# Performance work log

Hardware: AMD Instinct MI355X
Metric: run time of the kernel (lower is better)

The kernel has to match this reference:

```python
import jax, jax.numpy as jnp
import numpy as np

N_IN = 2048
N_OUT = 2048
RANK = 64
NUM_ITER = 4  # Newton-Schulz iterations, matches default num_iter=4


def setup_inputs() -> dict:
    key = jax.random.key(0)
    k1, k2, k3 = jax.random.split(key, 3)
    # scale U,V modestly so A = UV^T - VU^T is well-conditioned (mimics orthogonal init scale)
    scale = 1.0 / np.sqrt(N_IN)
    return {
        "input": jax.random.normal(k1, (8, 2048, N_IN), dtype=jnp.float32),
        "U": jax.random.normal(k2, (N_IN, RANK), dtype=jnp.float32) * scale,
        "V": jax.random.normal(k3, (N_IN, RANK), dtype=jnp.float32) * scale,
    }


def _orthogonal_weight(U, V):
    # A = U V^T - V U^T  (skew-symmetric, rank <= 2*rank)
    A = U @ V.T - V @ U.T              # [n, n]
    I = jnp.eye(N_IN, dtype=A.dtype)
    B = I - A
    X = I
    for _ in range(NUM_ITER):          # Newton-Schulz iteration for B^{-1}
        X = X @ (2.0 * I - B @ X)
    W_square = (I + A) @ X             # Cayley transform (I+A)(I-A)^{-1} approx
    return W_square[:N_OUT, :N_IN]


def reference(input, U, V):
    W = _orthogonal_weight(U, V)       # [out, in]
    # F.linear(input, W) = input @ W.T
    return jnp.einsum("bsi,oi->bso", input, W)
```

## Files before the change

### kernel.cpp

```cpp
#include <hip/hip_runtime.h>
#include <hip/hip_bf16.h>
#include <cstdint>
#include <cstddef>

#define NIN   2048
#define RANK  64
#define R2    128
#define NROWS 16384

typedef __bf16 bf16x8 __attribute__((ext_vector_type(8)));
typedef float  f32x4  __attribute__((ext_vector_type(4)));
typedef unsigned short u16x8 __attribute__((ext_vector_type(8)));

__device__ __forceinline__ unsigned short f2bf(float f) {
  union { float f; unsigned u; } x; x.f = f;
  return (unsigned short)((x.u + 0x7fffu + ((x.u >> 16) & 1u)) >> 16);
}

__global__ void k_zero(float* __restrict__ G) {
  G[blockIdx.x * 256 + threadIdx.x] = 0.f;
}

__global__ void k_prep(const float* __restrict__ U, const float* __restrict__ V,
                       unsigned short* __restrict__ Mf, float* __restrict__ G) {
  int b = blockIdx.x, tid = threadIdx.x;
  if (b < 128) {
    int CI = b * 256 + tid;
    int lane = CI & 63, J = (CI >> 6) & 63, t = CI >> 12;
    int n = t * 16 + (lane & 15);
    int k0 = J * 32 + (lane >> 4) * 8;
    const float* src = (n < RANK) ? (U + n) : (V + (n - RANK));
    u16x8 h;
#pragma unroll
    for (int e = 0; e < 8; ++e) h[e] = f2bf(src[(size_t)(k0 + e) * RANK]);
    *(u16x8*)(Mf + (size_t)CI * 8) = h;
  }
  int tile = b >> 3, ks = b & 7;
  int bi = tile >> 3, bj = tile & 7;
  int ty = tid >> 4, tx = tid & 15;
  int i = bi * 16 + ty, j = bj * 16 + tx;
  const float* Ai = (i < RANK) ? (U + i) : (V + (i - RANK));
  const float* Aj = (j < RANK) ? (U + j) : (V + (j - RANK));
  int k0 = ks * 256;
  float acc = 0.f;
#pragma unroll 8
  for (int k = k0; k < k0 + 256; ++k) acc += Ai[(size_t)k * RANK] * Aj[(size_t)k * RANK];
  if (i < RANK) atomicAdd(&G[(i + RANK) * R2 + j], -acc);
  else          atomicAdd(&G[(i - RANK) * R2 + j],  acc);
}

struct SOp { const float* A; const float* B; float* O; float a, b; };
struct SOps { SOp op[3]; };
__global__ void k_small(SOps ops) {
  SOp o = ops.op[blockIdx.x >> 6];
  int t = blockIdx.x & 63;
  int i = (t >> 3) * 16 + (threadIdx.x >> 4);
  int j = (t & 7) * 16 + (threadIdx.x & 15);
  float acc = 0.f;
#pragma unroll 8
  for (int k = 0; k < R2; ++k) {
    float av = o.A[i * R2 + k]; if (k == i) av += o.a;
    float bv = o.B[k * R2 + j]; if (k == j) bv += o.b;
    acc += av * bv;
  }
  o.O[i * R2 + j] = acc;
}

__global__ void k_D(const float* __restrict__ U, const float* __restrict__ V,
                    const float* __restrict__ H, const float* __restrict__ G15,
                    unsigned short* __restrict__ Df) {
  int idx = blockIdx.x * 256 + threadIdx.x;
  int i = idx >> 7, j = idx & 127;
  int jj = (j < RANK) ? (j + RANK) : (j - RANK);
  float sgn = (j < RANK) ? -1.f : 1.f;
  float acc = 0.f;
#pragma unroll 8
  for (int k = 0; k < R2; ++k) {
    float m = (k < RANK) ? U[(size_t)i * RANK + k] : V[(size_t)i * RANK + (k - RANK)];
    float t = 2.f * H[k * R2 + jj] - G15[k * R2 + jj];
    acc += m * (sgn * t);
  }
  int t_ = i >> 4, lr = i & 15;
  int J = j >> 5, lg = (j >> 3) & 3, e = j & 7;
  size_t CI = (size_t)(t_ * 4 + J) * 64 + lg * 16 + lr;
  Df[CI * 8 + e] = f2bf(acc);
}

__global__ __launch_bounds__(256) void k_T1(const float* __restrict__ input,
                                            const unsigned short* __restrict__ Mf,
                                            unsigned short* __restrict__ T1bf) {
  __shared__ __align__(16) unsigned char lds[73728];
  const int tid = threadIdx.x, lane = tid & 63, w = tid >> 6;
  const int lr = lane & 15, lg = lane >> 4;
  const int row0 = blockIdx.x * 32;
  unsigned char* abuf = lds + w * 8192;
  float* rbuf = (float*)lds;

  f32x4 acc[2][8] = {};
  const float* gbase = input + (size_t)row0 * NIN + w * 512;
  const int Jbase = w * 16;

  float4 s0[8], s1[8];
  bf16x8 bx[8], by[8];

#define T1_SLOAD(KT)                                                          \
  _Pragma("unroll") for (int p = 0; p < 8; ++p) {                             \
    int id = p * 64 + lane; int r = id >> 4, C = id & 15;                     \
    const float* g = gbase + (size_t)r * NIN + (KT) * 128 + C * 8;            \
    s0[p] = *(const float4*)g; s1[p] = *(const float4*)(g + 4);               \
  }
#define T1_SWRITE()                                                           \
  _Pragma("unroll") for (int p = 0; p < 8; ++p) {                             \
    int id = p * 64 + lane; int r = id >> 4, C = id & 15;                     \
    u16x8 h;                                                                  \
    h[0] = f2bf(s0[p].x); h[1] = f2bf(s0[p].y);                               \
    h[2] = f2bf(s0[p].z); h[3] = f2bf(s0[p].w);                               \
    h[4] = f2bf(s1[p].x); h[5] = f2bf(s1[p].y);                               \
    h[6] = f2bf(s1[p].z); h[7] = f2bf(s1[p].w);                               \
    *(u16x8*)(abuf + r * 256 + ((C ^ (r & 7)) << 4)) = h;                     \
  }
#define T1_BLOAD(P, S)                                                        \
  _Pragma("unroll") for (int t = 0; t < 8; ++t)                               \
    P[t] = *(const bf16x8*)(Mf + ((size_t)(t * 64 + Jbase + (S)) * 64 + lane) * 8);

  T1_SLOAD(0);
  T1_SWRITE();
  T1_BLOAD(bx, 0);

#pragma unroll
  for (int s = 0; s < 16; ++s) {
    const int kt = s >> 2, j = s & 3;
    if (j == 0 && kt < 3) { T1_SLOAD(kt + 1); }
    bf16x8 a0, a1;
    {
      int C = j * 4 + lg;
      a0 = *(const bf16x8*)(abuf + lr * 256 + ((C ^ (lr & 7)) << 4));
      a1 = *(const bf16x8*)(abuf + (16 + lr) * 256 + ((C ^ ((16 + lr) & 7)) << 4));
    }
    if (s < 15) { if (s & 1) { T1_BLOAD(bx, s + 1); } else { T1_BLOAD(by, s + 1); } }
#pragma unroll
    for (int t = 0; t < 8; ++t) {
      bf16x8 bcur = (s & 1) ? by[t] : bx[t];
      acc[0][t] = __builtin_amdgcn_mfma_f32_16x16x32_bf16(a0, bcur, acc[0][t], 0, 0, 0);
      acc[1][t] = __builtin_amdgcn_mfma_f32_16x16x32_bf16(a1, bcur, acc[1][t], 0, 0, 0);
    }
    if (j == 3 && kt < 3) { T1_SWRITE(); }
  }

  __syncthreads();
#pragma unroll
  for (int m = 0; m < 2; ++m)
#pragma unroll
    for (int t = 0; t < 8; ++t) {
      int col = t * 16 + lr, row = m * 16 + lg * 4;
      *(f32x4*)&rbuf[((size_t)w * 128 + col) * 36 + row] = acc[m][t];
    }
  __syncthreads();
  {
    int r = tid & 31, cg = tid >> 5;
    u16x8 o1, o2;
#pragma unroll
    for (int i = 0; i < 16; ++i) {
      int col = cg * 16 + i;
      float s = rbuf[(size_t)col * 36 + r]
              + rbuf[((size_t)128 + col) * 36 + r]
              + rbuf[((size_t)256 + col) * 36 + r]
              + rbuf[((size_t)384 + col) * 36 + r];
      if (i < 8) o1[i] = f2bf(s); else o2[i - 8] = f2bf(s);
    }
    unsigned short* dst = T1bf + (size_t)(row0 + r) * R2 + cg * 16;
    *(u16x8*)dst = o1;
    *(u16x8*)(dst + 8) = o2;
  }
}

__global__ __launch_bounds__(256) void k_OUT(const float* __restrict__ input,
                                             const unsigned short* __restrict__ T1bf,
                                             const unsigned short* __restrict__ Df,
                                             float* __restrict__ out) {
  __shared__ float obuf[4][32][132];
  const int tid = threadIdx.x, lane = tid & 63, w = tid >> 6;
  const int lr = lane & 15, lg = lane >> 4;
  const int row0 = blockIdx.x * 32;

  bf16x8 bq[2][4];
#pragma unroll
  for (int R = 0; R < 2; ++R)
#pragma unroll
    for (int J = 0; J < 4; ++J)
      bq[R][J] = *(const bf16x8*)(T1bf + (size_t)(row0 + R * 16 + lr) * R2 + J * 32 + lg * 8);

  bf16x8 xd[4], yd[4];
#define O_DLOAD(P, TTI)                                                       \
  _Pragma("unroll") for (int J = 0; J < 4; ++J)                               \
    P[J] = *(const bf16x8*)(Df + ((size_t)((w * 32 + (TTI)) * 4 + J) * 64 + lane) * 8);

  O_DLOAD(xd, 0);
#pragma unroll
  for (int g = 0; g < 4; ++g) {
#pragma unroll
    for (int tt = 0; tt < 8; ++tt) {
      const int tti = g * 8 + tt;
      if (tti < 31) { if (tti & 1) { O_DLOAD(xd, tti + 1); } else { O_DLOAD(yd, tti + 1); } }
#pragma unroll
      for (int R = 0; R < 2; ++R) {
        f32x4 o = {};
#pragma unroll
        for (int J = 0; J < 4; ++J) {
          bf16x8 d = (tti & 1) ? yd[J] : xd[J];
          o = __builtin_amdgcn_mfma_f32_16x16x32_bf16(d, bq[R][J], o, 0, 0, 0);
        }
        *(f32x4*)&obuf[w][R * 16 + lr][tt * 16 + lg * 4] = o;
      }
    }
#pragma unroll
    for (int c = 0; c < 16; ++c) {
      int id = c * 64 + lane;
      int r = id >> 5, cc = id & 31;
      f32x4 v = *(const f32x4*)&obuf[w][r][cc * 4];
      int grow = row0 + r, gcol = w * 512 + g * 128 + cc * 4;
      float4 inv = *(const float4*)(input + (size_t)grow * NIN + gcol);
      float4 res = { v[0] + inv.x, v[1] + inv.y, v[2] + inv.z, v[3] + inv.w };
      *(float4*)(out + (size_t)grow * NIN + gcol) = res;
    }
  }
}

extern "C" void kernel_launch(void* const* d_in, const int* in_sizes, int n_in,
                              void* d_out, int out_size, void* d_ws, size_t ws_size,
                              hipStream_t stream) {
  const float* input = (const float*)d_in[0];
  const float* U     = (const float*)d_in[1];
  const float* V     = (const float*)d_in[2];
  float* out = (float*)d_out;
  char* ws = (char*)d_ws;

  float* mats = (float*)ws;
  float* G   = mats + 0 * 16384;
  float* G2  = mats + 1 * 16384;
  float* G3  = mats + 2 * 16384;
  float* G4  = mats + 3 * 16384;
  float* G7  = mats + 4 * 16384;
  float* G8  = mats + 5 * 16384;
  float* H12 = mats + 6 * 16384;
  float* H124= mats + 7 * 16384;
  float* H   = mats + 8 * 16384;
  float* G15 = mats + 9 * 16384;
  unsigned short* Mf   = (unsigned short*)(ws + 10 * 65536);
  unsigned short* Df   = (unsigned short*)(ws + 10 * 65536 + 524288);
  unsigned short* T1bf = (unsigned short*)(ws + 10 * 65536 + 2 * 524288);

  k_zero<<<64, 256, 0, stream>>>(G);
  k_prep<<<512, 256, 0, stream>>>(U, V, Mf, G);
  k_T1<<<512, 256, 0, stream>>>(input, Mf, T1bf);

  { SOps o = {{ {G,  G,  G2, 0.f, 0.f}, {nullptr,nullptr,nullptr,0.f,0.f}, {nullptr,nullptr,nullptr,0.f,0.f} }};
    k_small<<<64, 256, 0, stream>>>(o); }
  { SOps o = {{ {G2, G2, G4, 0.f, 0.f}, {G2, G, G3, 0.f, 0.f}, {G, G2, H12, 1.f, 1.f} }};
    k_small<<<192, 256, 0, stream>>>(o); }
  { SOps o = {{ {G4, G4, G8, 0.f, 0.f}, {G3, G4, G7, 0.f, 0.f}, {H12, G4, H124, 0.f, 1.f} }};
    k_small<<<192, 256, 0, stream>>>(o); }
  { SOps o = {{ {G7, G8, G15, 0.f, 0.f}, {H124, G8, H, 0.f, 1.f}, {nullptr,nullptr,nullptr,0.f,0.f} }};
    k_small<<<128, 256, 0, stream>>>(o); }

  k_D<<<1024, 256, 0, stream>>>(U, V, H, G15, Df);
  k_OUT<<<512, 256, 0, stream>>>(input, T1bf, Df, out);
}
```

Before: 140.6 us.

## Fuse small-GEMM chain via grid barriers and merge T1 with output GEMM

```diff
diff --git a/kernel.cpp b/kernel.cpp
--- a/kernel.cpp
+++ b/kernel.cpp
@@ -17,8 +17,9 @@
   return (unsigned short)((x.u + 0x7fffu + ((x.u >> 16) & 1u)) >> 16);
 }
 
-__global__ void k_zero(float* __restrict__ G) {
+__global__ void k_zero(float* __restrict__ G, int* __restrict__ cnt) {
   G[blockIdx.x * 256 + threadIdx.x] = 0.f;
+  if (blockIdx.x == 0 && threadIdx.x < 8) cnt[threadIdx.x] = 0;
 }
 
 __global__ void k_prep(const float* __restrict__ U, const float* __restrict__ V,
@@ -49,46 +50,111 @@
   else          atomicAdd(&G[(i - RANK) * R2 + j],  acc);
 }
 
-struct SOp { const float* A; const float* B; float* O; float a, b; };
-struct SOps { SOp op[3]; };
-__global__ void k_small(SOps ops) {
-  SOp o = ops.op[blockIdx.x >> 6];
-  int t = blockIdx.x & 63;
-  int i = (t >> 3) * 16 + (threadIdx.x >> 4);
-  int j = (t & 7) * 16 + (threadIdx.x & 15);
+__device__ __forceinline__ void smallGemm(const float* __restrict__ A,
+                                          const float* __restrict__ B,
+                                          float* __restrict__ O,
+                                          float a, float b, int t, int tid) {
+  int i = (t >> 3) * 16 + (tid >> 4);
+  int j = (t & 7) * 16 + (tid & 15);
   float acc = 0.f;
 #pragma unroll 8
   for (int k = 0; k < R2; ++k) {
-    float av = o.A[i * R2 + k]; if (k == i) av += o.a;
-    float bv = o.B[k * R2 + j]; if (k == j) bv += o.b;
+    float av = A[i * R2 + k]; if (k == i) av += a;
+    float bv = B[k * R2 + j]; if (k == j) bv += b;
     acc += av * bv;
   }
-  o.O[i * R2 + j] = acc;
-}
-
-__global__ void k_D(const float* __restrict__ U, const float* __restrict__ V,
-                    const float* __restrict__ H, const float* __restrict__ G15,
-                    unsigned short* __restrict__ Df) {
-  int idx = blockIdx.x * 256 + threadIdx.x;
-  int i = idx >> 7, j = idx & 127;
-  int jj = (j < RANK) ? (j + RANK) : (j - RANK);
-  float sgn = (j < RANK) ? -1.f : 1.f;
-  float acc = 0.f;
-#pragma unroll 8
-  for (int k = 0; k < R2; ++k) {
-    float m = (k < RANK) ? U[(size_t)i * RANK + k] : V[(size_t)i * RANK + (k - RANK)];
-    float t = 2.f * H[k * R2 + jj] - G15[k * R2 + jj];
-    acc += m * (sgn * t);
-  }
-  int t_ = i >> 4, lr = i & 15;
-  int J = j >> 5, lg = (j >> 3) & 3, e = j & 7;
-  size_t CI = (size_t)(t_ * 4 + J) * 64 + lg * 16 + lr;
-  Df[CI * 8 + e] = f2bf(acc);
-}
-
-__global__ __launch_bounds__(256) void k_T1(const float* __restrict__ input,
-                                            const unsigned short* __restrict__ Mf,
-                                            unsigned short* __restrict__ T1bf) {
+  O[i * R2 + j] = acc;
+}
+
+__device__ __forceinline__ void gbar(int* c, int target, int tid) {
+  __syncthreads();
+  if (tid == 0) {
+    __threadfence();
+    __hip_atomic_fetch_add(c, 1, __ATOMIC_RELEASE, __HIP_MEMORY_SCOPE_AGENT);
+  }
+  while (__hip_atomic_load(c, __ATOMIC_ACQUIRE, __HIP_MEMORY_SCOPE_AGENT) < target)
+    __builtin_amdgcn_s_sleep(8);
+}
+
+__global__ __launch_bounds__(256) void k_chainD(const float* __restrict__ U,
+                                                const float* __restrict__ V,
+                                                float* __restrict__ mats,
+                                                unsigned short* __restrict__ Df,
+                                                int* __restrict__ cnt) {
+  __shared__ float elds[16384];
+  float* G_   = mats;
+  float* G2_  = mats + 1 * 16384;
+  float* G3_  = mats + 2 * 16384;
+  float* G4_  = mats + 3 * 16384;
+  float* G7_  = mats + 4 * 16384;
+  float* G8_  = mats + 5 * 16384;
+  float* H12_ = mats + 6 * 16384;
+  float* H124_= mats + 7 * 16384;
+  float* H_   = mats + 8 * 16384;
+  float* G15_ = mats + 9 * 16384;
+  const int cb = blockIdx.x, tid = threadIdx.x;
+
+  if (cb < 64) smallGemm(G_, G_, G2_, 0.f, 0.f, cb, tid);
+  gbar(&cnt[0], 192, tid);
+  { int op = cb >> 6, t = cb & 63;
+    if (op == 0)      smallGemm(G2_, G2_, G4_,  0.f, 0.f, t, tid);
+    else if (op == 1) smallGemm(G2_, G_,  G3_,  0.f, 0.f, t, tid);
+    else              smallGemm(G_,  G2_, H12_, 1.f, 1.f, t, tid); }
+  gbar(&cnt[1], 192, tid);
+  { int op = cb >> 6, t = cb & 63;
+    if (op == 0)      smallGemm(G4_,  G4_, G8_,   0.f, 0.f, t, tid);
+    else if (op == 1) smallGemm(G3_,  G4_, G7_,   0.f, 0.f, t, tid);
+    else              smallGemm(H12_, G4_, H124_, 0.f, 1.f, t, tid); }
+  gbar(&cnt[2], 192, tid);
+  if (cb < 128) {
+    int op = cb >> 6, t = cb & 63;
+    if (op == 0) smallGemm(G7_,   G8_, G15_, 0.f, 0.f, t, tid);
+    else         smallGemm(H124_, G8_, H_,   0.f, 1.f, t, tid);
+  }
+  gbar(&cnt[3], 192, tid);
+
+  if (cb < 128) {
+    const float4* H4 = (const float4*)H_;
+    const float4* X4 = (const float4*)G15_;
+#pragma unroll
+    for (int it = 0; it < 16; ++it) {
+      int i4 = it * 256 + tid;
+      float4 h = H4[i4], x = X4[i4];
+      float4 e = { 2.f*h.x - x.x, 2.f*h.y - x.y, 2.f*h.z - x.z, 2.f*h.w - x.w };
+      ((float4*)elds)[i4] = e;
+    }
+    __syncthreads();
+    int j = tid & 127, half = tid >> 7;
+    int jj = (j < RANK) ? (j + RANK) : (j - RANK);
+    float sgn = (j < RANK) ? -1.f : 1.f;
+    int i0 = cb * 16 + half * 8;
+    float acc[8] = {};
+#pragma unroll 4
+    for (int k = 0; k < RANK; ++k) {
+      float e = sgn * elds[k * R2 + jj];
+#pragma unroll
+      for (int rr = 0; rr < 8; ++rr) acc[rr] += U[(i0 + rr) * RANK + k] * e;
+    }
+#pragma unroll 4
+    for (int k = 0; k < RANK; ++k) {
+      float e = sgn * elds[(k + RANK) * R2 + jj];
+#pragma unroll
+      for (int rr = 0; rr < 8; ++rr) acc[rr] += V[(i0 + rr) * RANK + k] * e;
+    }
+#pragma unroll
+    for (int rr = 0; rr < 8; ++rr) {
+      int i = i0 + rr;
+      int t_ = i >> 4, lr = i & 15, J = j >> 5, lg = (j >> 3) & 3, e8 = j & 7;
+      size_t CI = (size_t)(t_ * 4 + J) * 64 + lg * 16 + lr;
+      Df[CI * 8 + e8] = f2bf(acc[rr]);
+    }
+  }
+}
+
+__global__ __launch_bounds__(256) void k_main(const float* __restrict__ input,
+                                              const unsigned short* __restrict__ Mf,
+                                              const unsigned short* __restrict__ Df,
+                                              float* __restrict__ out) {
   __shared__ __align__(16) unsigned char lds[73728];
   const int tid = threadIdx.x, lane = tid & 63, w = tid >> 6;
   const int lr = lane & 15, lg = lane >> 4;
@@ -99,7 +165,6 @@
   f32x4 acc[2][8] = {};
   const float* gbase = input + (size_t)row0 * NIN + w * 512;
   const int Jbase = w * 16;
-
   float4 s0[8], s1[8];
   bf16x8 bx[8], by[8];
 
@@ -126,7 +191,6 @@
   T1_SLOAD(0);
   T1_SWRITE();
   T1_BLOAD(bx, 0);
-
 #pragma unroll
   for (int s = 0; s < 16; ++s) {
     const int kt = s >> 2, j = s & 3;
@@ -158,38 +222,33 @@
   __syncthreads();
   {
     int r = tid & 31, cg = tid >> 5;
-    u16x8 o1, o2;
+    float sums[16];
 #pragma unroll
     for (int i = 0; i < 16; ++i) {
       int col = cg * 16 + i;
-      float s = rbuf[(size_t)col * 36 + r]
+      sums[i] = rbuf[(size_t)col * 36 + r]
               + rbuf[((size_t)128 + col) * 36 + r]
               + rbuf[((size_t)256 + col) * 36 + r]
               + rbuf[((size_t)384 + col) * 36 + r];
-      if (i < 8) o1[i] = f2bf(s); else o2[i - 8] = f2bf(s);
-    }
-    unsigned short* dst = T1bf + (size_t)(row0 + r) * R2 + cg * 16;
-    *(u16x8*)dst = o1;
-    *(u16x8*)(dst + 8) = o2;
-  }
-}
-
-__global__ __launch_bounds__(256) void k_OUT(const float* __restrict__ input,
-                                             const unsigned short* __restrict__ T1bf,
-                                             const unsigned short* __restrict__ Df,
-                                             float* __restrict__ out) {
-  __shared__ float obuf[4][32][132];
-  const int tid = threadIdx.x, lane = tid & 63, w = tid >> 6;
-  const int lr = lane & 15, lg = lane >> 4;
-  const int row0 = blockIdx.x * 32;
+    }
+    __syncthreads();
+    u16x8 o1, o2;
+#pragma unroll
+    for (int i = 0; i < 8; ++i) { o1[i] = f2bf(sums[i]); o2[i] = f2bf(sums[8 + i]); }
+    *(u16x8*)(lds + 65536 + r * 256 + (((cg * 2)     ^ (r & 7)) << 4)) = o1;
+    *(u16x8*)(lds + 65536 + r * 256 + (((cg * 2 + 1) ^ (r & 7)) << 4)) = o2;
+  }
+  __syncthreads();
 
   bf16x8 bq[2][4];
 #pragma unroll
   for (int R = 0; R < 2; ++R)
 #pragma unroll
-    for (int J = 0; J < 4; ++J)
-      bq[R][J] = *(const bf16x8*)(T1bf + (size_t)(row0 + R * 16 + lr) * R2 + J * 32 + lg * 8);
-
+    for (int J = 0; J < 4; ++J) {
+      int row = R * 16 + lr, cc = J * 4 + lg;
+      bq[R][J] = *(const bf16x8*)(lds + 65536 + row * 256 + ((cc ^ (row & 7)) << 4));
+    }
+  float* obufw = (float*)(lds + w * 8704);
   bf16x8 xd[4], yd[4];
 #define O_DLOAD(P, TTI)                                                       \
   _Pragma("unroll") for (int J = 0; J < 4; ++J)                               \
@@ -197,10 +256,10 @@
 
   O_DLOAD(xd, 0);
 #pragma unroll
-  for (int g = 0; g < 4; ++g) {
-#pragma unroll
-    for (int tt = 0; tt < 8; ++tt) {
-      const int tti = g * 8 + tt;
+  for (int g = 0; g < 8; ++g) {
+#pragma unroll
+    for (int tt = 0; tt < 4; ++tt) {
+      const int tti = g * 4 + tt;
       if (tti < 31) { if (tti & 1) { O_DLOAD(xd, tti + 1); } else { O_DLOAD(yd, tti + 1); } }
 #pragma unroll
       for (int R = 0; R < 2; ++R) {
@@ -210,15 +269,14 @@
           bf16x8 d = (tti & 1) ? yd[J] : xd[J];
           o = __builtin_amdgcn_mfma_f32_16x16x32_bf16(d, bq[R][J], o, 0, 0, 0);
         }
-        *(f32x4*)&obuf[w][R * 16 + lr][tt * 16 + lg * 4] = o;
+        *(f32x4*)&obufw[(R * 16 + lr) * 68 + tt * 16 + lg * 4] = o;
       }
     }
 #pragma unroll
-    for (int c = 0; c < 16; ++c) {
-      int id = c * 64 + lane;
-      int r = id >> 5, cc = id & 31;
-      f32x4 v = *(const f32x4*)&obuf[w][r][cc * 4];
-      int grow = row0 + r, gcol = w * 512 + g * 128 + cc * 4;
+    for (int c = 0; c < 8; ++c) {
+      int id = c * 64 + lane, r = id >> 4, cc = id & 15;
+      f32x4 v = *(const f32x4*)&obufw[r * 68 + cc * 4];
+      int grow = row0 + r, gcol = w * 512 + g * 64 + cc * 4;
       float4 inv = *(const float4*)(input + (size_t)grow * NIN + gcol);
       float4 res = { v[0] + inv.x, v[1] + inv.y, v[2] + inv.z, v[3] + inv.w };
       *(float4*)(out + (size_t)grow * NIN + gcol) = res;
@@ -236,33 +294,13 @@
   char* ws = (char*)d_ws;
 
   float* mats = (float*)ws;
-  float* G   = mats + 0 * 16384;
-  float* G2  = mats + 1 * 16384;
-  float* G3  = mats + 2 * 16384;
-  float* G4  = mats + 3 * 16384;
-  float* G7  = mats + 4 * 16384;
-  float* G8  = mats + 5 * 16384;
-  float* H12 = mats + 6 * 16384;
-  float* H124= mats + 7 * 16384;
-  float* H   = mats + 8 * 16384;
-  float* G15 = mats + 9 * 16384;
-  unsigned short* Mf   = (unsigned short*)(ws + 10 * 65536);
-  unsigned short* Df   = (unsigned short*)(ws + 10 * 65536 + 524288);
-  unsigned short* T1bf = (unsigned short*)(ws + 10 * 65536 + 2 * 524288);
-
-  k_zero<<<64, 256, 0, stream>>>(G);
+  float* G = mats;
+  unsigned short* Mf = (unsigned short*)(ws + 10 * 65536);
+  unsigned short* Df = (unsigned short*)(ws + 10 * 65536 + 524288);
+  int* cnt = (int*)(ws + 10 * 65536 + 2 * 524288);
+
+  k_zero<<<64, 256, 0, stream>>>(G, cnt);
   k_prep<<<512, 256, 0, stream>>>(U, V, Mf, G);
-  k_T1<<<512, 256, 0, stream>>>(input, Mf, T1bf);
-
-  { SOps o = {{ {G,  G,  G2, 0.f, 0.f}, {nullptr,nullptr,nullptr,0.f,0.f}, {nullptr,nullptr,nullptr,0.f,0.f} }};
-    k_small<<<64, 256, 0, stream>>>(o); }
-  { SOps o = {{ {G2, G2, G4, 0.f, 0.f}, {G2, G, G3, 0.f, 0.f}, {G, G2, H12, 1.f, 1.f} }};
-    k_small<<<192, 256, 0, stream>>>(o); }
-  { SOps o = {{ {G4, G4, G8, 0.f, 0.f}, {G3, G4, G7, 0.f, 0.f}, {H12, G4, H124, 0.f, 1.f} }};
-    k_small<<<192, 256, 0, stream>>>(o); }
-  { SOps o = {{ {G7, G8, G15, 0.f, 0.f}, {H124, G8, H, 0.f, 1.f}, {nullptr,nullptr,nullptr,0.f,0.f} }};
-    k_small<<<128, 256, 0, stream>>>(o); }
-
-  k_D<<<1024, 256, 0, stream>>>(U, V, H, G15, Df);
-  k_OUT<<<512, 256, 0, stream>>>(input, T1bf, Df, out);
-}
+  k_chainD<<<192, 256, 0, stream>>>(U, V, mats, Df, cnt);
+  k_main<<<512, 256, 0, stream>>>(input, Mf, Df, out);
+}
```

Result: slower. 242.1 us (+72.3%).
